# Kernel optimization log

Hardware: AMD Instinct MI355X
Metric: run time of the kernel (lower is better)

The kernel has to match this reference:

```python
import math
import jax, jax.numpy as jnp
import numpy as np

N, L, C, H, E = 50000, 3, 64, 4, 800000
D = C // H


def setup_inputs() -> dict:
    key = jax.random.key(0)
    ks = jax.random.split(key, 10)
    s = 1.0 / math.sqrt(C)
    return {
        "history": jax.random.normal(ks[0], (N, L, C), dtype=jnp.float32),
        "edge_index": jax.random.randint(ks[1], (2, E), 0, N, dtype=jnp.int32),
        "Wq": jax.random.normal(ks[2], (C, C), dtype=jnp.float32) * s,
        "bq": jnp.zeros((C,), dtype=jnp.float32),
        "Wk": jax.random.normal(ks[3], (C, C), dtype=jnp.float32) * s,
        "bk": jnp.zeros((C,), dtype=jnp.float32),
        "Wv": jax.random.normal(ks[4], (C, C), dtype=jnp.float32) * s,
        "bv": jnp.zeros((C,), dtype=jnp.float32),
        "Wo": jax.random.normal(ks[5], (C, C), dtype=jnp.float32) * s,
        "bo": jnp.zeros((C,), dtype=jnp.float32),
    }


def reference(history, edge_index, Wq, bq, Wk, bk, Wv, bv, Wo, bo):
    row, col = edge_index[0], edge_index[1]
    current = history[:, -1]                                   # [N, C]
    # torch Linear: y = x @ W.T + b
    q = (current @ Wq.T + bq).reshape(N, H, D)                  # [N, H, D]
    k = (history @ Wk.T + bk).reshape(N, L, H, D)               # [N, L, H, D]
    v = (history @ Wv.T + bv).reshape(N, L, H, D)

    q_dst = q[col][:, None]                                     # [E, 1, H, D]
    k_src = k[row]                                              # [E, L, H, D]
    scores = (q_dst * k_src).sum(-1) / math.sqrt(D)             # [E, L, H]
    token_w = jax.nn.softmax(scores, axis=1)                    # layer attention
    edge_msg = (token_w[..., None] * v[row]).sum(axis=1)        # [E, H, D]

    # edge_softmax over incoming edges of each destination node (per head)
    edge_scores = scores.max(axis=1)                            # [E, H]
    seg_max = jax.ops.segment_max(edge_scores, col, num_segments=N)
    seg_max = jnp.where(jnp.isfinite(seg_max), seg_max, 0.0)
    e = jnp.exp(edge_scores - seg_max[col])                     # [E, H]
    denom = jax.ops.segment_sum(e, col, num_segments=N)         # [N, H]
    edge_w = e / denom[col]                                     # [E, H]

    out = jnp.zeros((N, H, D), dtype=current.dtype)
    out = out.at[col].add(edge_msg * edge_w[..., None])          # scatter-add
    out = out.reshape(N, C)
    return out @ Wo.T + bo + current
```

## Files before the change

### kernel.cpp

```cpp
#include <hip/hip_runtime.h>

#define DEV __device__ __forceinline__

constexpr int L = 3;
constexpr int C = 64;
constexpr int H = 4;
constexpr int CAP = 64;

typedef unsigned short ushort8v __attribute__((ext_vector_type(8)));
typedef unsigned short ushort4v __attribute__((ext_vector_type(4)));
typedef short short8v __attribute__((ext_vector_type(8)));
typedef float f32x4 __attribute__((ext_vector_type(4)));

DEV float4 ld4g(const float* p) { return *reinterpret_cast<const float4*>(p); }
DEV float b2f(unsigned short u) {
    union { float f; unsigned int i; } x; x.i = ((unsigned int)u) << 16; return x.f;
}
DEV unsigned short f2b(float f) {
    unsigned int u = __float_as_uint(f);
    return (unsigned short)((u + 0x7FFFu + ((u >> 16) & 1u)) >> 16);
}
DEV float dot8(float4 a, float4 b, ushort8v k) {
    return a.x*b2f(k[0]) + a.y*b2f(k[1]) + a.z*b2f(k[2]) + a.w*b2f(k[3])
         + b.x*b2f(k[4]) + b.y*b2f(k[5]) + b.z*b2f(k[6]) + b.w*b2f(k[7]);
}
DEV void acc8(float4& A, float4& B, float w, ushort8v v) {
    A.x = fmaf(w, b2f(v[0]), A.x); A.y = fmaf(w, b2f(v[1]), A.y);
    A.z = fmaf(w, b2f(v[2]), A.z); A.w = fmaf(w, b2f(v[3]), A.w);
    B.x = fmaf(w, b2f(v[4]), B.x); B.y = fmaf(w, b2f(v[5]), B.y);
    B.z = fmaf(w, b2f(v[6]), B.z); B.w = fmaf(w, b2f(v[7]), B.w);
}

__global__ __launch_bounds__(256) void prep_kernel(
    const float* __restrict__ Wk, const float* __restrict__ Wv,
    const float* __restrict__ Wq, const float* __restrict__ Wo,
    unsigned short* __restrict__ Wf)
{
    const int tid = threadIdx.x;
    #pragma unroll
    for (int j = 0; j < 16; ++j) {
        int idx = tid + (j << 8);
        int c = idx >> 6, k = idx & 63;
        int fp = (k >> 3) * 512 + c * 8 + (k & 7);
        Wf[fp]            = f2b(Wk[idx]);
        Wf[4096 + fp]     = f2b(Wv[idx]);
        Wf[8192 + fp]     = f2b(Wq[idx] * 0.25f);
        int gp = (c << 6) | ((((k >> 2) ^ c) & 15) << 2) | (k & 3);
        Wf[12288 + gp]    = f2b(Wo[idx]);
    }
}

__global__ __launch_bounds__(256) void qkv_kernel(
    const float* __restrict__ history,
    const unsigned short* __restrict__ Wf,
    const float* __restrict__ bk, const float* __restrict__ bv,
    const float* __restrict__ bq,
    unsigned short* __restrict__ kvout, unsigned short* __restrict__ qout,
    const int* __restrict__ ei, int* __restrict__ counts,
    unsigned short* __restrict__ srcs,
    int N, int E, int nkvBlocks)
{
    __shared__ __align__(16) unsigned short WL[2][4096];
    __shared__ __align__(16) unsigned short ST[4][2048];

    {
        int gid = blockIdx.x * 256 + threadIdx.x;
        if (gid < E) {
            int c = ei[E + gid];
            int r = atomicAdd(&counts[c], 1);
            if (r < CAP) srcs[c * CAP + r] = (unsigned short)ei[gid];
        }
    }

    const bool isKV = (int)blockIdx.x < nkvBlocks;
    const int nqBlocks = (N + 63) / 64;
    if (!isKV && (int)blockIdx.x >= nkvBlocks + nqBlocks) return;
    const int rowBase = (isKV ? blockIdx.x : (blockIdx.x - nkvBlocks)) * 64;
    const int totalRows = isKV ? N * L : N;
    const int tid = threadIdx.x;

    {
        int o = tid << 4;
        if (isKV) {
            *(ushort8v*)&WL[0][o]     = *(const ushort8v*)&Wf[o];
            *(ushort8v*)&WL[0][o + 8] = *(const ushort8v*)&Wf[o + 8];
            *(ushort8v*)&WL[1][o]     = *(const ushort8v*)&Wf[4096 + o];
            *(ushort8v*)&WL[1][o + 8] = *(const ushort8v*)&Wf[4096 + o + 8];
        } else {
            *(ushort8v*)&WL[0][o]     = *(const ushort8v*)&Wf[8192 + o];
            *(ushort8v*)&WL[0][o + 8] = *(const ushort8v*)&Wf[8192 + o + 8];
        }
    }
    __syncthreads();

    const int lane = tid & 63;
    const int wid = tid >> 6;
    const int rbase = rowBase + wid * 16;
    const int kg = lane >> 4;
    const int kbase = kg << 3;
    const int bcol = lane & 15;

    const int arow = min(rbase + (lane & 15), totalRows - 1);
    const size_t srcRow = isKV ? (size_t)arow : ((size_t)arow * L + (L - 1));
    const float* xp = &history[srcRow * C];
    float4 xa = ld4g(xp + kbase), xb = ld4g(xp + kbase + 4);
    float4 xc = ld4g(xp + 32 + kbase), xd = ld4g(xp + 32 + kbase + 4);
    short8v a0, a1;
    a0[0] = (short)f2b(xa.x); a0[1] = (short)f2b(xa.y);
    a0[2] = (short)f2b(xa.z); a0[3] = (short)f2b(xa.w);
    a0[4] = (short)f2b(xb.x); a0[5] = (short)f2b(xb.y);
    a0[6] = (short)f2b(xb.z); a0[7] = (short)f2b(xb.w);
    a1[0] = (short)f2b(xc.x); a1[1] = (short)f2b(xc.y);
    a1[2] = (short)f2b(xc.z); a1[3] = (short)f2b(xc.w);
    a1[4] = (short)f2b(xd.x); a1[5] = (short)f2b(xd.y);
    a1[6] = (short)f2b(xd.z); a1[7] = (short)f2b(xd.w);

    const f32x4 zero = {0.f, 0.f, 0.f, 0.f};

    if (isKV) {
        f32x4 aK[4] = {zero, zero, zero, zero};
        f32x4 aV[4] = {zero, zero, zero, zero};
        #pragma unroll
        for (int ct = 0; ct < 4; ++ct) {
            int col = ct * 16 + bcol;
            short8v bk0 = *(const short8v*)&WL[0][(kg) * 512 + col * 8];
            short8v bk1 = *(const short8v*)&WL[0][(4 + kg) * 512 + col * 8];
            short8v bv0 = *(const short8v*)&WL[1][(kg) * 512 + col * 8];
            short8v bv1 = *(const short8v*)&WL[1][(4 + kg) * 512 + col * 8];
            aK[ct] = __builtin_amdgcn_mfma_f32_16x16x32_bf16(a0, bk0, aK[ct], 0, 0, 0);
            aK[ct] = __builtin_amdgcn_mfma_f32_16x16x32_bf16(a1, bk1, aK[ct], 0, 0, 0);
            aV[ct] = __builtin_amdgcn_mfma_f32_16x16x32_bf16(a0, bv0, aV[ct], 0, 0, 0);
            aV[ct] = __builtin_amdgcn_mfma_f32_16x16x32_bf16(a1, bv1, aV[ct], 0, 0, 0);
        }
        unsigned short* st = &ST[wid][0];
        #pragma unroll
        for (int ct = 0; ct < 4; ++ct) {
            int col = ct * 16 + bcol;
            float biasK = bk[col];
            float biasV = bv[col];
            #pragma unroll
            for (int i = 0; i < 4; ++i) {
                int r = kg * 4 + i;
                int ck = col, cv = 64 + col;
                int pk = r * 128 + ((((ck >> 3) ^ r) & 15) << 3) + (ck & 7);
                int pv = r * 128 + ((((cv >> 3) ^ r) & 15) << 3) + (cv & 7);
                st[pk] = f2b(aK[ct][i] + biasK);
                st[pv] = f2b(aV[ct][i] + biasV);
            }
        }
        asm volatile("s_waitcnt lgkmcnt(0)" ::: "memory");
        unsigned short* base = kvout + (size_t)rbase * 128;
        #pragma unroll
        for (int i = 0; i < 4; ++i) {
            int chunk = i * 64 + lane;
            int r = chunk >> 4;
            int cc = chunk & 15;
            if (rbase + r < totalRows) {
                ushort8v vls = *(const ushort8v*)&st[(r * 16 + ((cc ^ r) & 15)) * 8];
                *(ushort8v*)(base + chunk * 8) = vls;
            }
        }
    } else {
        f32x4 aQ[4] = {zero, zero, zero, zero};
        #pragma unroll
        for (int ct = 0; ct < 4; ++ct) {
            int col = ct * 16 + bcol;
            short8v bq0 = *(const short8v*)&WL[0][(kg) * 512 + col * 8];
            short8v bq1 = *(const short8v*)&WL[0][(4 + kg) * 512 + col * 8];
            aQ[ct] = __builtin_amdgcn_mfma_f32_16x16x32_bf16(a0, bq0, aQ[ct], 0, 0, 0);
            aQ[ct] = __builtin_amdgcn_mfma_f32_16x16x32_bf16(a1, bq1, aQ[ct], 0, 0, 0);
        }
        unsigned short* st = &ST[wid][0];
        #pragma unroll
        for (int ct = 0; ct < 4; ++ct) {
            int col = ct * 16 + bcol;
            float bias = bq[col] * 0.25f;
            #pragma unroll
            for (int i = 0; i < 4; ++i) {
                int r = kg * 4 + i;
                int p = r * 64 + ((((col >> 3) ^ r) & 7) << 3) + (col & 7);
                st[p] = f2b(aQ[ct][i] + bias);
            }
        }
        asm volatile("s_waitcnt lgkmcnt(0)" ::: "memory");
        unsigned short* baseq = qout + (size_t)rbase * 64;
        #pragma unroll
        for (int i = 0; i < 2; ++i) {
            int chunk = i * 64 + lane;
            int r = chunk >> 3;
            int cc = chunk & 7;
            if (rbase + r < totalRows) {
                ushort8v vq = *(const ushort8v*)&st[(r * 8 + ((cc ^ r) & 7)) * 8];
                *(ushort8v*)(baseq + chunk * 8) = vq;
            }
        }
    }
}

__global__ __launch_bounds__(256) void gather_kernel(
    const unsigned short* __restrict__ srcs, const int* __restrict__ counts,
    const unsigned short* __restrict__ q, const unsigned short* __restrict__ kv,
    const float* __restrict__ history,
    const unsigned short* __restrict__ Wf, const float* __restrict__ bo,
    float* __restrict__ out, int N)
{
    __shared__ __align__(16) unsigned short WoS[4096];
    __shared__ float boS[64];
    __shared__ float sc4[4][64];

    const int tid = threadIdx.x;
    {
        int o = tid << 4;
        *(ushort8v*)&WoS[o]     = *(const ushort8v*)&Wf[12288 + o];
        *(ushort8v*)&WoS[o + 8] = *(const ushort8v*)&Wf[12288 + o + 8];
    }
    if (tid < 64) boS[tid] = bo[tid];
    __syncthreads();

    const int n = blockIdx.x * 4 + (tid >> 6);
    if (n >= N) return;
    const int lane = tid & 63;
    const int wid = tid >> 6;
    float* sc = &sc4[wid][0];

    const int sub = lane >> 3;
    const int ld = lane & 7;
    const int c0 = ld << 3;
    const int wrow = lane << 6;

    const int start = n * CAP;
    const int cnt = min(counts[n], CAP);

    const float xv = history[((size_t)n * L + (L - 1)) * C + lane];
    ushort8v q8 = *(const ushort8v*)&q[(size_t)n * C + c0];
    float4 qa, qb;
    qa.x = b2f(q8[0]); qa.y = b2f(q8[1]); qa.z = b2f(q8[2]); qa.w = b2f(q8[3]);
    qb.x = b2f(q8[4]); qb.y = b2f(q8[5]); qb.z = b2f(q8[6]); qb.w = b2f(q8[7]);
    float4 ma = make_float4(0.f, 0.f, 0.f, 0.f);
    float4 mb = make_float4(0.f, 0.f, 0.f, 0.f);
    float dsum = 0.f;

    for (int i = sub; i < cnt; i += 8) {
        const int src = srcs[start + i];
        const unsigned short* kb = kv + (size_t)src * (L * 2 * C) + c0;
        ushort8v k0 = *(const ushort8v*)(kb);
        ushort8v k1 = *(const ushort8v*)(kb + 2 * C);
        ushort8v k2 = *(const ushort8v*)(kb + 4 * C);

        float s0 = dot8(qa, qb, k0);
        float s1 = dot8(qa, qb, k1);
        float s2 = dot8(qa, qb, k2);
        s0 += __shfl_xor(s0, 1);
        s1 += __shfl_xor(s1, 1);
        s2 += __shfl_xor(s2, 1);

        float e0 = __expf(s0), e1 = __expf(s1), e2 = __expf(s2);
        float ee = fmaxf(fmaxf(e0, e1), e2);
        float scl = ee / (e0 + e1 + e2);
        float w0 = e0 * scl, w1 = e1 * scl, w2 = e2 * scl;

        ushort8v v0 = *(const ushort8v*)(kb + C);
        ushort8v v1 = *(const ushort8v*)(kb + 3 * C);
        ushort8v v2 = *(const ushort8v*)(kb + 5 * C);
        acc8(ma, mb, w0, v0);
        acc8(ma, mb, w1, v1);
        acc8(ma, mb, w2, v2);
        dsum += ee;
    }

    #pragma unroll
    for (int m = 8; m <= 32; m <<= 1) {
        ma.x += __shfl_xor(ma.x, m); ma.y += __shfl_xor(ma.y, m);
        ma.z += __shfl_xor(ma.z, m); ma.w += __shfl_xor(ma.w, m);
        mb.x += __shfl_xor(mb.x, m); mb.y += __shfl_xor(mb.y, m);
        mb.z += __shfl_xor(mb.z, m); mb.w += __shfl_xor(mb.w, m);
        dsum += __shfl_xor(dsum, m);
    }

    if (sub == 0) {
        float inv = dsum > 0.f ? 1.f / dsum : 0.f;
        float4 oa, ob;
        oa.x = ma.x * inv; oa.y = ma.y * inv; oa.z = ma.z * inv; oa.w = ma.w * inv;
        ob.x = mb.x * inv; ob.y = mb.y * inv; ob.z = mb.z * inv; ob.w = mb.w * inv;
        *(float4*)&sc[c0] = oa;
        *(float4*)&sc[c0 + 4] = ob;
    }
    asm volatile("s_waitcnt lgkmcnt(0)" ::: "memory");
    float oc = boS[lane] + xv;
    #pragma unroll
    for (int j = 0; j < 16; ++j) {
        float4 aj = *(const float4*)&sc[j << 2];
        ushort4v w = *(const ushort4v*)&WoS[wrow | (((j ^ lane) & 15) << 2)];
        oc += aj.x * b2f(w[0]) + aj.y * b2f(w[1])
            + aj.z * b2f(w[2]) + aj.w * b2f(w[3]);
    }
    out[(size_t)n * C + lane] = oc;
}

extern "C" void kernel_launch(void* const* d_in, const int* in_sizes, int n_in,
                              void* d_out, int out_size, void* d_ws, size_t ws_size,
                              hipStream_t stream)
{
    const float* history = (const float*)d_in[0];
    const int*   ei      = (const int*)d_in[1];
    const float* Wq = (const float*)d_in[2];
    const float* bq = (const float*)d_in[3];
    const float* Wk = (const float*)d_in[4];
    const float* bk = (const float*)d_in[5];
    const float* Wv = (const float*)d_in[6];
    const float* bv = (const float*)d_in[7];
    const float* Wo = (const float*)d_in[8];
    const float* bo = (const float*)d_in[9];
    const int N = in_sizes[0] / (L * C);
    const int E = in_sizes[1] / 2;

    unsigned short* Wf    = (unsigned short*)d_ws;
    unsigned short* qbuf  = Wf + 4 * 4096;
    unsigned short* kvbuf = qbuf + (size_t)N * C;
    int* counts = (int*)(kvbuf + (size_t)N * L * 2 * C);
    unsigned short* srcs  = (unsigned short*)(counts + N);

    hipMemsetAsync(counts, 0, (size_t)N * sizeof(int), stream);

    prep_kernel<<<1, 256, 0, stream>>>(Wk, Wv, Wq, Wo, Wf);

    const int nkv = (N * L + 63) / 64;
    const int nq  = (N + 63) / 64;
    const int eb  = (E + 255) / 256;
    int qkvBlocks = nkv + nq;
    if (qkvBlocks < eb) qkvBlocks = eb;
    qkv_kernel<<<qkvBlocks, 256, 0, stream>>>(history, Wf, bk, bv, bq,
                                              kvbuf, qbuf, ei, counts, srcs,
                                              N, E, nkv);

    gather_kernel<<<(N + 3) / 4, 256, 0, stream>>>(srcs, counts, qbuf, kvbuf,
                                                   history, Wf, bo,
                                                   (float*)d_out, N);
}
```

Before: 150.0 us.

## Compute Q alongside K/V per row, fold memset into prep, raise gather priority

```diff
diff --git a/kernel.cpp b/kernel.cpp
--- a/kernel.cpp
+++ b/kernel.cpp
@@ -34,19 +34,24 @@
 __global__ __launch_bounds__(256) void prep_kernel(
     const float* __restrict__ Wk, const float* __restrict__ Wv,
     const float* __restrict__ Wq, const float* __restrict__ Wo,
-    unsigned short* __restrict__ Wf)
+    unsigned short* __restrict__ Wf, int* __restrict__ counts, int N)
 {
     const int tid = threadIdx.x;
-    #pragma unroll
-    for (int j = 0; j < 16; ++j) {
-        int idx = tid + (j << 8);
-        int c = idx >> 6, k = idx & 63;
-        int fp = (k >> 3) * 512 + c * 8 + (k & 7);
-        Wf[fp]            = f2b(Wk[idx]);
-        Wf[4096 + fp]     = f2b(Wv[idx]);
-        Wf[8192 + fp]     = f2b(Wq[idx] * 0.25f);
-        int gp = (c << 6) | ((((k >> 2) ^ c) & 15) << 2) | (k & 3);
-        Wf[12288 + gp]    = f2b(Wo[idx]);
+    if (blockIdx.x == 0) {
+        #pragma unroll
+        for (int j = 0; j < 16; ++j) {
+            int idx = tid + (j << 8);
+            int c = idx >> 6, k = idx & 63;
+            int fp = (k >> 3) * 512 + c * 8 + (k & 7);
+            Wf[fp]            = f2b(Wk[idx]);
+            Wf[4096 + fp]     = f2b(Wv[idx]);
+            Wf[8192 + fp]     = f2b(Wq[idx] * 0.25f);
+            int gp = (c << 6) | ((((k >> 2) ^ c) & 15) << 2) | (k & 3);
+            Wf[12288 + gp]    = f2b(Wo[idx]);
+        }
+    } else {
+        int gid = (blockIdx.x - 1) * 256 + tid;
+        if (gid < N) counts[gid] = 0;
     }
 }
 
@@ -58,38 +63,32 @@
     unsigned short* __restrict__ kvout, unsigned short* __restrict__ qout,
     const int* __restrict__ ei, int* __restrict__ counts,
     unsigned short* __restrict__ srcs,
-    int N, int E, int nkvBlocks)
+    int N, int E)
 {
-    __shared__ __align__(16) unsigned short WL[2][4096];
+    __shared__ __align__(16) unsigned short WL[3][4096];
     __shared__ __align__(16) unsigned short ST[4][2048];
 
     {
-        int gid = blockIdx.x * 256 + threadIdx.x;
-        if (gid < E) {
+        const int stride = gridDim.x * 256;
+        for (int gid = blockIdx.x * 256 + threadIdx.x; gid < E; gid += stride) {
             int c = ei[E + gid];
             int r = atomicAdd(&counts[c], 1);
             if (r < CAP) srcs[c * CAP + r] = (unsigned short)ei[gid];
         }
     }
 
-    const bool isKV = (int)blockIdx.x < nkvBlocks;
-    const int nqBlocks = (N + 63) / 64;
-    if (!isKV && (int)blockIdx.x >= nkvBlocks + nqBlocks) return;
-    const int rowBase = (isKV ? blockIdx.x : (blockIdx.x - nkvBlocks)) * 64;
-    const int totalRows = isKV ? N * L : N;
+    const int rowBase = blockIdx.x * 64;
+    const int totalRows = N * L;
     const int tid = threadIdx.x;
 
     {
         int o = tid << 4;
-        if (isKV) {
-            *(ushort8v*)&WL[0][o]     = *(const ushort8v*)&Wf[o];
-            *(ushort8v*)&WL[0][o + 8] = *(const ushort8v*)&Wf[o + 8];
-            *(ushort8v*)&WL[1][o]     = *(const ushort8v*)&Wf[4096 + o];
-            *(ushort8v*)&WL[1][o + 8] = *(const ushort8v*)&Wf[4096 + o + 8];
-        } else {
-            *(ushort8v*)&WL[0][o]     = *(const ushort8v*)&Wf[8192 + o];
-            *(ushort8v*)&WL[0][o + 8] = *(const ushort8v*)&Wf[8192 + o + 8];
-        }
+        *(ushort8v*)&WL[0][o]     = *(const ushort8v*)&Wf[o];
+        *(ushort8v*)&WL[0][o + 8] = *(const ushort8v*)&Wf[o + 8];
+        *(ushort8v*)&WL[1][o]     = *(const ushort8v*)&Wf[4096 + o];
+        *(ushort8v*)&WL[1][o + 8] = *(const ushort8v*)&Wf[4096 + o + 8];
+        *(ushort8v*)&WL[2][o]     = *(const ushort8v*)&Wf[8192 + o];
+        *(ushort8v*)&WL[2][o + 8] = *(const ushort8v*)&Wf[8192 + o + 8];
     }
     __syncthreads();
 
@@ -101,8 +100,7 @@
     const int bcol = lane & 15;
 
     const int arow = min(rbase + (lane & 15), totalRows - 1);
-    const size_t srcRow = isKV ? (size_t)arow : ((size_t)arow * L + (L - 1));
-    const float* xp = &history[srcRow * C];
+    const float* xp = &history[(size_t)arow * C];
     float4 xa = ld4g(xp + kbase), xb = ld4g(xp + kbase + 4);
     float4 xc = ld4g(xp + 32 + kbase), xd = ld4g(xp + 32 + kbase + 4);
     short8v a0, a1;
@@ -116,83 +114,63 @@
     a1[6] = (short)f2b(xd.z); a1[7] = (short)f2b(xd.w);
 
     const f32x4 zero = {0.f, 0.f, 0.f, 0.f};
-
-    if (isKV) {
-        f32x4 aK[4] = {zero, zero, zero, zero};
-        f32x4 aV[4] = {zero, zero, zero, zero};
-        #pragma unroll
-        for (int ct = 0; ct < 4; ++ct) {
-            int col = ct * 16 + bcol;
-            short8v bk0 = *(const short8v*)&WL[0][(kg) * 512 + col * 8];
-            short8v bk1 = *(const short8v*)&WL[0][(4 + kg) * 512 + col * 8];
-            short8v bv0 = *(const short8v*)&WL[1][(kg) * 512 + col * 8];
-            short8v bv1 = *(const short8v*)&WL[1][(4 + kg) * 512 + col * 8];
-            aK[ct] = __builtin_amdgcn_mfma_f32_16x16x32_bf16(a0, bk0, aK[ct], 0, 0, 0);
-            aK[ct] = __builtin_amdgcn_mfma_f32_16x16x32_bf16(a1, bk1, aK[ct], 0, 0, 0);
-            aV[ct] = __builtin_amdgcn_mfma_f32_16x16x32_bf16(a0, bv0, aV[ct], 0, 0, 0);
-            aV[ct] = __builtin_amdgcn_mfma_f32_16x16x32_bf16(a1, bv1, aV[ct], 0, 0, 0);
-        }
-        unsigned short* st = &ST[wid][0];
-        #pragma unroll
-        for (int ct = 0; ct < 4; ++ct) {
-            int col = ct * 16 + bcol;
-            float biasK = bk[col];
-            float biasV = bv[col];
-            #pragma unroll
-            for (int i = 0; i < 4; ++i) {
-                int r = kg * 4 + i;
-                int ck = col, cv = 64 + col;
-                int pk = r * 128 + ((((ck >> 3) ^ r) & 15) << 3) + (ck & 7);
-                int pv = r * 128 + ((((cv >> 3) ^ r) & 15) << 3) + (cv & 7);
-                st[pk] = f2b(aK[ct][i] + biasK);
-                st[pv] = f2b(aV[ct][i] + biasV);
-            }
-        }
-        asm volatile("s_waitcnt lgkmcnt(0)" ::: "memory");
-        unsigned short* base = kvout + (size_t)rbase * 128;
+    f32x4 aK[4] = {zero, zero, zero, zero};
+    f32x4 aV[4] = {zero, zero, zero, zero};
+    f32x4 aQ[4] = {zero, zero, zero, zero};
+    #pragma unroll
+    for (int ct = 0; ct < 4; ++ct) {
+        int col = ct * 16 + bcol;
+        short8v bk0 = *(const short8v*)&WL[0][(kg) * 512 + col * 8];
+        short8v bk1 = *(const short8v*)&WL[0][(4 + kg) * 512 + col * 8];
+        short8v bv0 = *(const short8v*)&WL[1][(kg) * 512 + col * 8];
+        short8v bv1 = *(const short8v*)&WL[1][(4 + kg) * 512 + col * 8];
+        short8v bq0 = *(const short8v*)&WL[2][(kg) * 512 + col * 8];
+        short8v bq1 = *(const short8v*)&WL[2][(4 + kg) * 512 + col * 8];
+        aK[ct] = __builtin_amdgcn_mfma_f32_16x16x32_bf16(a0, bk0, aK[ct], 0, 0, 0);
+        aK[ct] = __builtin_amdgcn_mfma_f32_16x16x32_bf16(a1, bk1, aK[ct], 0, 0, 0);
+        aV[ct] = __builtin_amdgcn_mfma_f32_16x16x32_bf16(a0, bv0, aV[ct], 0, 0, 0);
+        aV[ct] = __builtin_amdgcn_mfma_f32_16x16x32_bf16(a1, bv1, aV[ct], 0, 0, 0);
+        aQ[ct] = __builtin_amdgcn_mfma_f32_16x16x32_bf16(a0, bq0, aQ[ct], 0, 0, 0);
+        aQ[ct] = __builtin_amdgcn_mfma_f32_16x16x32_bf16(a1, bq1, aQ[ct], 0, 0, 0);
+    }
+
+    unsigned short* st = &ST[wid][0];
+    #pragma unroll
+    for (int ct = 0; ct < 4; ++ct) {
+        int col = ct * 16 + bcol;
+        float biasK = bk[col];
+        float biasV = bv[col];
         #pragma unroll
         for (int i = 0; i < 4; ++i) {
-            int chunk = i * 64 + lane;
-            int r = chunk >> 4;
-            int cc = chunk & 15;
-            if (rbase + r < totalRows) {
-                ushort8v vls = *(const ushort8v*)&st[(r * 16 + ((cc ^ r) & 15)) * 8];
-                *(ushort8v*)(base + chunk * 8) = vls;
-            }
-        }
-    } else {
-        f32x4 aQ[4] = {zero, zero, zero, zero};
+            int r = kg * 4 + i;
+            int ck = col, cv = 64 + col;
+            int pk = r * 128 + ((((ck >> 3) ^ r) & 15) << 3) + (ck & 7);
+            int pv = r * 128 + ((((cv >> 3) ^ r) & 15) << 3) + (cv & 7);
+            st[pk] = f2b(aK[ct][i] + biasK);
+            st[pv] = f2b(aV[ct][i] + biasV);
+        }
+    }
+    #pragma unroll
+    for (int ct = 0; ct < 4; ++ct) {
+        int col = ct * 16 + bcol;
+        float biasQ = bq[col] * 0.25f;
         #pragma unroll
-        for (int ct = 0; ct < 4; ++ct) {
-            int col = ct * 16 + bcol;
-            short8v bq0 = *(const short8v*)&WL[0][(kg) * 512 + col * 8];
-            short8v bq1 = *(const short8v*)&WL[0][(4 + kg) * 512 + col * 8];
-            aQ[ct] = __builtin_amdgcn_mfma_f32_16x16x32_bf16(a0, bq0, aQ[ct], 0, 0, 0);
-            aQ[ct] = __builtin_amdgcn_mfma_f32_16x16x32_bf16(a1, bq1, aQ[ct], 0, 0, 0);
-        }
-        unsigned short* st = &ST[wid][0];
-        #pragma unroll
-        for (int ct = 0; ct < 4; ++ct) {
-            int col = ct * 16 + bcol;
-            float bias = bq[col] * 0.25f;
-            #pragma unroll
-            for (int i = 0; i < 4; ++i) {
-                int r = kg * 4 + i;
-                int p = r * 64 + ((((col >> 3) ^ r) & 7) << 3) + (col & 7);
-                st[p] = f2b(aQ[ct][i] + bias);
-            }
-        }
-        asm volatile("s_waitcnt lgkmcnt(0)" ::: "memory");
-        unsigned short* baseq = qout + (size_t)rbase * 64;
-        #pragma unroll
-        for (int i = 0; i < 2; ++i) {
-            int chunk = i * 64 + lane;
-            int r = chunk >> 3;
-            int cc = chunk & 7;
-            if (rbase + r < totalRows) {
-                ushort8v vq = *(const ushort8v*)&st[(r * 8 + ((cc ^ r) & 7)) * 8];
-                *(ushort8v*)(baseq + chunk * 8) = vq;
-            }
+        for (int i = 0; i < 4; ++i) {
+            int grow = rbase + kg * 4 + i;
+            if (grow < totalRows && (grow % 3) == 2)
+                qout[(size_t)(grow / 3) * C + col] = f2b(aQ[ct][i] + biasQ);
+        }
+    }
+    asm volatile("s_waitcnt lgkmcnt(0)" ::: "memory");
+    unsigned short* base = kvout + (size_t)rbase * 128;
+    #pragma unroll
+    for (int i = 0; i < 4; ++i) {
+        int chunk = i * 64 + lane;
+        int r = chunk >> 4;
+        int cc = chunk & 15;
+        if (rbase + r < totalRows) {
+            ushort8v vls = *(const ushort8v*)&st[(r * 16 + ((cc ^ r) & 15)) * 8];
+            *(ushort8v*)(base + chunk * 8) = vls;
         }
     }
 }
@@ -240,6 +218,7 @@
     float4 mb = make_float4(0.f, 0.f, 0.f, 0.f);
     float dsum = 0.f;
 
+    __builtin_amdgcn_s_setprio(1);
     for (int i = sub; i < cnt; i += 8) {
         const int src = srcs[start + i];
         const unsigned short* kb = kv + (size_t)src * (L * 2 * C) + c0;
@@ -267,6 +246,7 @@
         acc8(ma, mb, w2, v2);
         dsum += ee;
     }
+    __builtin_amdgcn_s_setprio(0);
 
     #pragma unroll
     for (int m = 8; m <= 32; m <<= 1) {
@@ -320,18 +300,12 @@
     int* counts = (int*)(kvbuf + (size_t)N * L * 2 * C);
     unsigned short* srcs  = (unsigned short*)(counts + N);
 
-    hipMemsetAsync(counts, 0, (size_t)N * sizeof(int), stream);
-
-    prep_kernel<<<1, 256, 0, stream>>>(Wk, Wv, Wq, Wo, Wf);
+    const int sb = (N + 255) / 256;
+    prep_kernel<<<sb + 1, 256, 0, stream>>>(Wk, Wv, Wq, Wo, Wf, counts, N);
 
     const int nkv = (N * L + 63) / 64;
-    const int nq  = (N + 63) / 64;
-    const int eb  = (E + 255) / 256;
-    int qkvBlocks = nkv + nq;
-    if (qkvBlocks < eb) qkvBlocks = eb;
-    qkv_kernel<<<qkvBlocks, 256, 0, stream>>>(history, Wf, bk, bv, bq,
-                                              kvbuf, qbuf, ei, counts, srcs,
-                                              N, E, nkv);
+    qkv_kernel<<<nkv, 256, 0, stream>>>(history, Wf, bk, bv, bq,
+                                        kvbuf, qbuf, ei, counts, srcs, N, E);
 
     gather_kernel<<<(N + 3) / 4, 256, 0, stream>>>(srcs, counts, qbuf, kvbuf,
                                                    history, Wf, bo,
```

Result: no change. 150.1 us (+0.1%).
